# Kernel optimization log

Hardware: AMD Instinct MI355X
Metric: run time of the kernel (lower is better)

The kernel has to match this reference:

```python
import jax, jax.numpy as jnp
import numpy as np

EPS = 1e-9
ROUTING_ITERATIONS = 3


def setup_inputs() -> dict:
    key = jax.random.key(0)
    k1, k2 = jax.random.split(key)
    B, Nin, Din = 32, 2048, 16   # batch, input capsules, input capsule dim
    Nout, Dout = 64, 32          # output capsules, output capsule dim
    x = jax.random.normal(k1, (B, Nin, Din), dtype=jnp.float32)
    # transformation weights W[i, j, d, k] (shared across batch)
    W = jax.random.normal(k2, (Nin, Nout, Dout, Din), dtype=jnp.float32) * 0.05
    bias = jnp.zeros((Nout, Dout), dtype=jnp.float32)
    return {"x": x, "W": W, "bias": bias}


def _squash(s):
    # squash along last axis (capsule vector dim)
    sq_norm = jnp.sum(jnp.square(s), axis=-1, keepdims=True)
    scale = sq_norm / (1.0 + sq_norm)
    return scale * s / jnp.sqrt(sq_norm + EPS)


def reference(x, W, bias):
    # u_hat[b,i,j,d] = sum_k W[i,j,d,k] * x[b,i,k]
    u_hat = jnp.einsum('ijdk,bik->bijd', W, x)
    B, Nin, Nout, Dout = u_hat.shape
    b_log = jnp.zeros((B, Nin, Nout), dtype=u_hat.dtype)  # routing logits
    v = None
    for it in range(ROUTING_ITERATIONS):
        c = jax.nn.softmax(b_log, axis=2)                 # coupling coeffs over Nout
        s = jnp.einsum('bij,bijd->bjd', c, u_hat) + bias  # [B, Nout, Dout]
        v = _squash(s)
        if it < ROUTING_ITERATIONS - 1:
            b_log = b_log + jnp.einsum('bijd,bjd->bij', u_hat, v)
    return v  # [B, Nout, Dout]
```

## Files before the change

### kernel.cpp

```cpp
#include <hip/hip_runtime.h>
#include <hip/hip_bf16.h>
#include <stdint.h>


#define CB    32
#define NIN   2048
#define DIN   16
#define NOUT  64
#define DOUT  32
#define IPB   8
#define NCB   (NIN / IPB)
#define WI    (NOUT * DOUT * DIN)
#define WELEM ((size_t)NIN * WI)

typedef __attribute__((ext_vector_type(8)))  short bf16x8;
typedef __attribute__((ext_vector_type(16))) float f32x16;
typedef _Float16 h2 __attribute__((ext_vector_type(2)));

#define VOFF 0
#define COFF 135168
#define XOFF_IT 143616
#define SMEM_IT  153856
#define SMEM_P0  10240

static __device__ __forceinline__ uint32_t pack_bf2(float a, float b) {
    __hip_bfloat162 hh = __float22bfloat162_rn(make_float2(a, b));
    uint32_t u; __builtin_memcpy(&u, &hh, 4); return u;
}
static __device__ __forceinline__ uint16_t f2bf(float v) {
    return (uint16_t)(pack_bf2(v, 0.f) & 0xffffu);
}
static __device__ __forceinline__ float bf2f(uint16_t u) {
    uint32_t v = (uint32_t)u << 16; float f; __builtin_memcpy(&f, &v, 4); return f;
}
static __device__ __forceinline__ uint32_t pack_h2(float a, float b) {
    h2 r; r.x = (_Float16)a; r.y = (_Float16)b;
    uint32_t u; __builtin_memcpy(&u, &r, 4); return u;
}
static __device__ __forceinline__ h2 as_h2(uint32_t u) {
    h2 r; __builtin_memcpy(&r, &u, 4); return r;
}

template <int IT>
__global__ __launch_bounds__(1024, 4) void caps_pass(
    const float* __restrict__ x, const void* __restrict__ Wv,
    uint32_t* __restrict__ WhOut,
    const float* __restrict__ v_prev, const float* __restrict__ blog_in,
    float* __restrict__ blog_out, uint16_t* __restrict__ s_partial)
{
    extern __shared__ char smem[];
    uint32_t* v_lds = (uint32_t*)(smem + VOFF);
    float*    c_lds = (float*)(smem + COFF);
    uint32_t* x_lds = (uint32_t*)(smem + (IT > 0 ? XOFF_IT : 0));

    const int cb = blockIdx.x;
    const int t  = threadIdx.x;
    const int w  = t >> 6, l = t & 63;
    const int bl = l & 31, h = l >> 5;
    const int j0 = w * 4;

    {
        const int b = t >> 5, i = (t >> 2) & 7, k4 = (t & 3) * 4;
        const float4 xv = *(const float4*)(x + ((size_t)b * NIN + cb * IPB + i) * DIN + k4);
        x_lds[(i * 32 + b) * 10 + (k4 >> 1)]     = pack_bf2(xv.x, xv.y);
        x_lds[(i * 32 + b) * 10 + (k4 >> 1) + 1] = pack_bf2(xv.z, xv.w);
    }
    if (IT > 0) {
#pragma unroll 4
        for (int rep = 0; rep < 32; ++rep) {
            const int idx = rep * 1024 + t;
            const int b = idx >> 10, j = (idx >> 4) & 63, dp = idx & 15;
            const float2 vv = *(const float2*)(v_prev + ((size_t)b * NOUT + j) * DOUT + dp * 2);
            v_lds[(j * 16 + dp) * 33 + b] = pack_h2(vv.x, vv.y);
        }
    }
    __syncthreads();

    f32x16 sacc[4];
#pragma unroll
    for (int jj = 0; jj < 4; ++jj) sacc[jj] = (f32x16)0.0f;

    const uint16_t* Wb = (const uint16_t*)Wv;
    const float*    Wf = (const float*)Wv;
    constexpr int base_dp[8] = {0, 1, 4, 5, 8, 9, 12, 13};

#pragma unroll 1
    for (int i = 0; i < IPB; ++i) {
        const int ig = cb * IPB + i;
        const size_t wbase = (size_t)ig * WI;

        bf16x8 bfr;
        {
            uint32_t uu[4];
            const uint32_t* xp = &x_lds[(i * 32 + bl) * 10 + h * 4];
            uu[0] = xp[0]; uu[1] = xp[1]; uu[2] = xp[2]; uu[3] = xp[3];
            __builtin_memcpy(&bfr, uu, 16);
        }

        if (IT > 0) {
#pragma unroll
            for (int jj = 0; jj < 4; ++jj) {
                const int j = j0 + jj;
                const bf16x8 afr = *(const bf16x8*)(Wb + wbase + (size_t)(j * 32 + bl) * 16 + h * 8);
                const f32x16 D = __builtin_amdgcn_mfma_f32_32x32x16_bf16(afr, bfr, (f32x16)0.0f, 0, 0, 0);
                float acc = 0.f;
#pragma unroll
                for (int rp = 0; rp < 8; ++rp) {
                    const int dp = base_dp[rp] + 2 * h;
                    h2 dpk; dpk.x = (_Float16)D[2 * rp]; dpk.y = (_Float16)D[2 * rp + 1];
                    acc = __builtin_amdgcn_fdot2(dpk, as_h2(v_lds[(j * 16 + dp) * 33 + bl]), acc, false);
                }
                acc += __shfl_xor(acc, 32);
                if (h == 0) c_lds[j * 33 + bl] = acc;
            }
            __syncthreads();

#pragma unroll
            for (int rr = 0; rr < 2; ++rr) {
                const int b = w * 2 + rr;
                float bv = c_lds[l * 33 + b];
                if (IT == 2) bv += blog_in[((size_t)b * NIN + ig) * NOUT + l];
                if (IT == 1) blog_out[((size_t)b * NIN + ig) * NOUT + l] = bv;
                float m = bv;
#pragma unroll
                for (int o = 32; o; o >>= 1) m = fmaxf(m, __shfl_xor(m, o));
                const float e = __expf(bv - m);
                float s = e;
#pragma unroll
                for (int o = 32; o; o >>= 1) s += __shfl_xor(s, o);
                c_lds[l * 33 + b] = e / s;
            }
            __syncthreads();
        }

#pragma unroll
        for (int jj = 0; jj < 4; ++jj) {
            const int j = j0 + jj;
            if (IT == 0) {
                const float4* wp = (const float4*)(Wf + wbase + (size_t)(j * 32 + bl) * 16 + h * 8);
                const float4 a4 = wp[0], b4 = wp[1];
                uint32_t uu[4];
                uu[0] = pack_bf2(a4.x, a4.y); uu[1] = pack_bf2(a4.z, a4.w);
                uu[2] = pack_bf2(b4.x, b4.y); uu[3] = pack_bf2(b4.z, b4.w);
                bf16x8 afr; __builtin_memcpy(&afr, uu, 16);
                uint4 st; st.x = uu[0]; st.y = uu[1]; st.z = uu[2]; st.w = uu[3];
                *(uint4*)(WhOut + ((wbase + (size_t)(j * 32 + bl) * 16 + h * 8) >> 1)) = st;
                sacc[jj] = __builtin_amdgcn_mfma_f32_32x32x16_bf16(afr, bfr, sacc[jj], 0, 0, 0);
            } else {
                const bf16x8 afr = *(const bf16x8*)(Wb + wbase + (size_t)(j * 32 + bl) * 16 + h * 8);
                const f32x16 D = __builtin_amdgcn_mfma_f32_32x32x16_bf16(afr, bfr, (f32x16)0.0f, 0, 0, 0);
                const float cv = c_lds[j * 33 + bl];
                sacc[jj] += D * cv;
            }
        }
        if (IT > 0) __syncthreads();
    }

    const float cscale = (IT == 0) ? (1.0f / 64.0f) : 1.0f;
#pragma unroll
    for (int jj = 0; jj < 4; ++jj) {
        const int j = j0 + jj;
#pragma unroll
        for (int r = 0; r < 16; ++r) {
            const int d = (r & 3) + 8 * (r >> 2) + 4 * h;
            s_partial[(size_t)cb * (2048 * 32) + (size_t)(j * 32 + d) * 32 + bl] =
                f2bf(sacc[jj][r] * cscale);
        }
    }
}

__global__ __launch_bounds__(256) void caps_squash(
    const uint16_t* __restrict__ sp, const float* __restrict__ bias,
    float* __restrict__ vout)
{
    const int j  = blockIdx.x >> 2;
    const int bq = blockIdx.x & 3;
    const int t  = threadIdx.x;
    const int d  = t >> 3;
    const int blq = t & 7;
    const int b  = bq * 8 + blq;

    const uint16_t* p = sp + (size_t)(j * 32 + d) * 32 + b;
    float s0 = 0.f, s1 = 0.f, s2 = 0.f, s3 = 0.f;
#pragma unroll 4
    for (int c = 0; c < NCB; c += 4) {
        s0 += bf2f(p[(size_t)(c + 0) * (2048 * 32)]);
        s1 += bf2f(p[(size_t)(c + 1) * (2048 * 32)]);
        s2 += bf2f(p[(size_t)(c + 2) * (2048 * 32)]);
        s3 += bf2f(p[(size_t)(c + 3) * (2048 * 32)]);
    }
    const float sv = ((s0 + s1) + (s2 + s3)) + bias[j * DOUT + d];

    float sq = sv * sv;
    sq += __shfl_xor(sq, 8);
    sq += __shfl_xor(sq, 16);
    sq += __shfl_xor(sq, 32);

    __shared__ float sh[4][8];
    if ((t & 63) < 8) sh[t >> 6][t & 7] = sq;
    __syncthreads();
    const float tot = sh[0][blq] + sh[1][blq] + sh[2][blq] + sh[3][blq];
    const float scale = (tot / (1.0f + tot)) * rsqrtf(tot + 1e-9f);
    vout[(size_t)b * (NOUT * DOUT) + j * DOUT + d] = scale * sv;
}

extern "C" void kernel_launch(void* const* d_in, const int* in_sizes, int n_in,
                              void* d_out, int out_size, void* d_ws, size_t ws_size,
                              hipStream_t stream) {
    const float* x    = (const float*)d_in[0];
    const float* W    = (const float*)d_in[1];
    const float* bias = (const float*)d_in[2];
    float* out = (float*)d_out;

    char* base = (char*)d_ws;
    uint32_t* Wh    = (uint32_t*)base;
    float*    blog  = (float*)(base + WELEM * 2);
    uint16_t* spart = (uint16_t*)(base + WELEM * 2 + (size_t)CB * NIN * NOUT * 4);
    float*    vbuf  = (float*)(base + WELEM * 2 + (size_t)CB * NIN * NOUT * 4
                               + (size_t)NCB * 2048 * 32 * 2);
    (void)ws_size;

    hipFuncSetAttribute(reinterpret_cast<const void*>(caps_pass<0>),
                        hipFuncAttributeMaxDynamicSharedMemorySize, SMEM_P0);
    hipFuncSetAttribute(reinterpret_cast<const void*>(caps_pass<1>),
                        hipFuncAttributeMaxDynamicSharedMemorySize, SMEM_IT);
    hipFuncSetAttribute(reinterpret_cast<const void*>(caps_pass<2>),
                        hipFuncAttributeMaxDynamicSharedMemorySize, SMEM_IT);

    caps_pass<0><<<NCB, 1024, SMEM_P0, stream>>>(x, W, Wh, nullptr, nullptr, nullptr, spart);
    caps_squash<<<NOUT * 4, 256, 0, stream>>>(spart, bias, vbuf);

    caps_pass<1><<<NCB, 1024, SMEM_IT, stream>>>(x, Wh, nullptr, vbuf, nullptr, blog, spart);
    caps_squash<<<NOUT * 4, 256, 0, stream>>>(spart, bias, vbuf);

    caps_pass<2><<<NCB, 1024, SMEM_IT, stream>>>(x, Wh, nullptr, vbuf, blog, nullptr, spart);
    caps_squash<<<NOUT * 4, 256, 0, stream>>>(spart, bias, out);
}
```

Measured before the change: 249.2 us.

## Restructure routing passes into phased agreement, batched softmax, and scaled-x MFMA

Splits the templated pass into a separate first-pass kernel and a routing-iteration kernel. The iteration kernel now keeps v in registers instead of a large LDS table. It computes agreement logits for all 8 input capsules before doing a single softmax phase, which replaces the three barriers per input capsule with two in total. The weighted sum folds the coupling coefficient into the x operand (c*x in bf16), so the MFMA accumulates directly instead of doing a separate D*c multiply. LDS use drops from about 150KB to about 78KB, which may allow more blocks per CU. In exchange, the bf16 weights are read twice per block and rounding c*x to bf16 adds precision error.

```diff
diff --git a/kernel.cpp b/kernel.cpp
--- a/kernel.cpp
+++ b/kernel.cpp
@@ -17,11 +17,9 @@
 typedef __attribute__((ext_vector_type(16))) float f32x16;
 typedef _Float16 h2 __attribute__((ext_vector_type(2)));
 
-#define VOFF 0
-#define COFF 135168
-#define XOFF_IT 143616
-#define SMEM_IT  153856
-#define SMEM_P0  10240
+#define XOFF_IT 67584
+#define SMEM_IT 77824
+#define SMEM_P0 10240
 
 static __device__ __forceinline__ uint32_t pack_bf2(float a, float b) {
     __hip_bfloat162 hh = __float22bfloat162_rn(make_float2(a, b));
@@ -40,18 +38,19 @@
 static __device__ __forceinline__ h2 as_h2(uint32_t u) {
     h2 r; __builtin_memcpy(&r, &u, 4); return r;
 }
-
-template <int IT>
-__global__ __launch_bounds__(1024, 4) void caps_pass(
-    const float* __restrict__ x, const void* __restrict__ Wv,
-    uint32_t* __restrict__ WhOut,
-    const float* __restrict__ v_prev, const float* __restrict__ blog_in,
-    float* __restrict__ blog_out, uint16_t* __restrict__ s_partial)
+static __device__ __forceinline__ float bflo(uint32_t u) {
+    uint32_t v = u << 16; float f; __builtin_memcpy(&f, &v, 4); return f;
+}
+static __device__ __forceinline__ float bfhi(uint32_t u) {
+    uint32_t v = u & 0xffff0000u; float f; __builtin_memcpy(&f, &v, 4); return f;
+}
+
+__global__ __launch_bounds__(1024, 4) void caps_pass0(
+    const float* __restrict__ x, const float* __restrict__ Wf,
+    uint32_t* __restrict__ WhOut, uint16_t* __restrict__ s_partial)
 {
     extern __shared__ char smem[];
-    uint32_t* v_lds = (uint32_t*)(smem + VOFF);
-    float*    c_lds = (float*)(smem + COFF);
-    uint32_t* x_lds = (uint32_t*)(smem + (IT > 0 ? XOFF_IT : 0));
+    uint32_t* x_lds = (uint32_t*)smem;
 
     const int cb = blockIdx.x;
     const int t  = threadIdx.x;
@@ -65,30 +64,15 @@
         x_lds[(i * 32 + b) * 10 + (k4 >> 1)]     = pack_bf2(xv.x, xv.y);
         x_lds[(i * 32 + b) * 10 + (k4 >> 1) + 1] = pack_bf2(xv.z, xv.w);
     }
-    if (IT > 0) {
-#pragma unroll 4
-        for (int rep = 0; rep < 32; ++rep) {
-            const int idx = rep * 1024 + t;
-            const int b = idx >> 10, j = (idx >> 4) & 63, dp = idx & 15;
-            const float2 vv = *(const float2*)(v_prev + ((size_t)b * NOUT + j) * DOUT + dp * 2);
-            v_lds[(j * 16 + dp) * 33 + b] = pack_h2(vv.x, vv.y);
-        }
-    }
     __syncthreads();
 
     f32x16 sacc[4];
 #pragma unroll
     for (int jj = 0; jj < 4; ++jj) sacc[jj] = (f32x16)0.0f;
-
-    const uint16_t* Wb = (const uint16_t*)Wv;
-    const float*    Wf = (const float*)Wv;
-    constexpr int base_dp[8] = {0, 1, 4, 5, 8, 9, 12, 13};
 
 #pragma unroll 1
     for (int i = 0; i < IPB; ++i) {
-        const int ig = cb * IPB + i;
-        const size_t wbase = (size_t)ig * WI;
-
+        const size_t wbase = (size_t)(cb * IPB + i) * WI;
         bf16x8 bfr;
         {
             uint32_t uu[4];
@@ -96,67 +80,22 @@
             uu[0] = xp[0]; uu[1] = xp[1]; uu[2] = xp[2]; uu[3] = xp[3];
             __builtin_memcpy(&bfr, uu, 16);
         }
-
-        if (IT > 0) {
-#pragma unroll
-            for (int jj = 0; jj < 4; ++jj) {
-                const int j = j0 + jj;
-                const bf16x8 afr = *(const bf16x8*)(Wb + wbase + (size_t)(j * 32 + bl) * 16 + h * 8);
-                const f32x16 D = __builtin_amdgcn_mfma_f32_32x32x16_bf16(afr, bfr, (f32x16)0.0f, 0, 0, 0);
-                float acc = 0.f;
-#pragma unroll
-                for (int rp = 0; rp < 8; ++rp) {
-                    const int dp = base_dp[rp] + 2 * h;
-                    h2 dpk; dpk.x = (_Float16)D[2 * rp]; dpk.y = (_Float16)D[2 * rp + 1];
-                    acc = __builtin_amdgcn_fdot2(dpk, as_h2(v_lds[(j * 16 + dp) * 33 + bl]), acc, false);
-                }
-                acc += __shfl_xor(acc, 32);
-                if (h == 0) c_lds[j * 33 + bl] = acc;
-            }
-            __syncthreads();
-
-#pragma unroll
-            for (int rr = 0; rr < 2; ++rr) {
-                const int b = w * 2 + rr;
-                float bv = c_lds[l * 33 + b];
-                if (IT == 2) bv += blog_in[((size_t)b * NIN + ig) * NOUT + l];
-                if (IT == 1) blog_out[((size_t)b * NIN + ig) * NOUT + l] = bv;
-                float m = bv;
-#pragma unroll
-                for (int o = 32; o; o >>= 1) m = fmaxf(m, __shfl_xor(m, o));
-                const float e = __expf(bv - m);
-                float s = e;
-#pragma unroll
-                for (int o = 32; o; o >>= 1) s += __shfl_xor(s, o);
-                c_lds[l * 33 + b] = e / s;
-            }
-            __syncthreads();
-        }
-
 #pragma unroll
         for (int jj = 0; jj < 4; ++jj) {
             const int j = j0 + jj;
-            if (IT == 0) {
-                const float4* wp = (const float4*)(Wf + wbase + (size_t)(j * 32 + bl) * 16 + h * 8);
-                const float4 a4 = wp[0], b4 = wp[1];
-                uint32_t uu[4];
-                uu[0] = pack_bf2(a4.x, a4.y); uu[1] = pack_bf2(a4.z, a4.w);
-                uu[2] = pack_bf2(b4.x, b4.y); uu[3] = pack_bf2(b4.z, b4.w);
-                bf16x8 afr; __builtin_memcpy(&afr, uu, 16);
-                uint4 st; st.x = uu[0]; st.y = uu[1]; st.z = uu[2]; st.w = uu[3];
-                *(uint4*)(WhOut + ((wbase + (size_t)(j * 32 + bl) * 16 + h * 8) >> 1)) = st;
-                sacc[jj] = __builtin_amdgcn_mfma_f32_32x32x16_bf16(afr, bfr, sacc[jj], 0, 0, 0);
-            } else {
-                const bf16x8 afr = *(const bf16x8*)(Wb + wbase + (size_t)(j * 32 + bl) * 16 + h * 8);
-                const f32x16 D = __builtin_amdgcn_mfma_f32_32x32x16_bf16(afr, bfr, (f32x16)0.0f, 0, 0, 0);
-                const float cv = c_lds[j * 33 + bl];
-                sacc[jj] += D * cv;
-            }
-        }
-        if (IT > 0) __syncthreads();
-    }
-
-    const float cscale = (IT == 0) ? (1.0f / 64.0f) : 1.0f;
+            const size_t eoff = wbase + (size_t)(j * 32 + bl) * 16 + h * 8;
+            const float4* wp = (const float4*)(Wf + eoff);
+            const float4 a4 = wp[0], b4 = wp[1];
+            uint32_t uu[4];
+            uu[0] = pack_bf2(a4.x, a4.y); uu[1] = pack_bf2(a4.z, a4.w);
+            uu[2] = pack_bf2(b4.x, b4.y); uu[3] = pack_bf2(b4.z, b4.w);
+            bf16x8 afr; __builtin_memcpy(&afr, uu, 16);
+            uint4 st; st.x = uu[0]; st.y = uu[1]; st.z = uu[2]; st.w = uu[3];
+            *(uint4*)(WhOut + (eoff >> 1)) = st;
+            sacc[jj] = __builtin_amdgcn_mfma_f32_32x32x16_bf16(afr, bfr, sacc[jj], 0, 0, 0);
+        }
+    }
+
 #pragma unroll
     for (int jj = 0; jj < 4; ++jj) {
         const int j = j0 + jj;
@@ -164,7 +103,127 @@
         for (int r = 0; r < 16; ++r) {
             const int d = (r & 3) + 8 * (r >> 2) + 4 * h;
             s_partial[(size_t)cb * (2048 * 32) + (size_t)(j * 32 + d) * 32 + bl] =
-                f2bf(sacc[jj][r] * cscale);
+                f2bf(sacc[jj][r] * (1.0f / 64.0f));
+        }
+    }
+}
+
+template <int IT>
+__global__ __launch_bounds__(1024, 4) void caps_it(
+    const float* __restrict__ x, const uint16_t* __restrict__ Wh,
+    const float* __restrict__ v_prev, const float* __restrict__ blog_in,
+    float* __restrict__ blog_out, uint16_t* __restrict__ s_partial)
+{
+    extern __shared__ char smem[];
+    float*    c_lds = (float*)smem;
+    uint32_t* x_lds = (uint32_t*)(smem + XOFF_IT);
+
+    const int cb = blockIdx.x;
+    const int t  = threadIdx.x;
+    const int w  = t >> 6, l = t & 63;
+    const int bl = l & 31, h = l >> 5;
+    const int j0 = w * 4;
+
+    {
+        const int b = t >> 5, i = (t >> 2) & 7, k4 = (t & 3) * 4;
+        const float4 xv = *(const float4*)(x + ((size_t)b * NIN + cb * IPB + i) * DIN + k4);
+        x_lds[(i * 32 + b) * 10 + (k4 >> 1)]     = pack_bf2(xv.x, xv.y);
+        x_lds[(i * 32 + b) * 10 + (k4 >> 1) + 1] = pack_bf2(xv.z, xv.w);
+    }
+
+    constexpr int base_dp[8] = {0, 1, 4, 5, 8, 9, 12, 13};
+    uint32_t vreg[4][8];
+#pragma unroll
+    for (int jj = 0; jj < 4; ++jj)
+#pragma unroll
+        for (int rp = 0; rp < 8; ++rp) {
+            const int d0 = 2 * (base_dp[rp] + 2 * h);
+            const float2 vv = *(const float2*)(v_prev
+                + ((size_t)bl * NOUT + j0 + jj) * DOUT + d0);
+            vreg[jj][rp] = pack_h2(vv.x, vv.y);
+        }
+    __syncthreads();
+
+#pragma unroll 2
+    for (int i = 0; i < IPB; ++i) {
+        const size_t wbase = (size_t)(cb * IPB + i) * WI;
+        bf16x8 bfr;
+        {
+            uint32_t uu[4];
+            const uint32_t* xp = &x_lds[(i * 32 + bl) * 10 + h * 4];
+            uu[0] = xp[0]; uu[1] = xp[1]; uu[2] = xp[2]; uu[3] = xp[3];
+            __builtin_memcpy(&bfr, uu, 16);
+        }
+#pragma unroll
+        for (int jj = 0; jj < 4; ++jj) {
+            const int j = j0 + jj;
+            const bf16x8 afr = *(const bf16x8*)(Wh + wbase + (size_t)(j * 32 + bl) * 16 + h * 8);
+            const f32x16 D = __builtin_amdgcn_mfma_f32_32x32x16_bf16(afr, bfr, (f32x16)0.0f, 0, 0, 0);
+            float acc = 0.f;
+#pragma unroll
+            for (int rp = 0; rp < 8; ++rp) {
+                h2 dpk; dpk.x = (_Float16)D[2 * rp]; dpk.y = (_Float16)D[2 * rp + 1];
+                acc = __builtin_amdgcn_fdot2(dpk, as_h2(vreg[jj][rp]), acc, false);
+            }
+            acc += __shfl_xor(acc, 32);
+            if (h == 0) c_lds[(i * 64 + j) * 33 + bl] = acc;
+        }
+    }
+    __syncthreads();
+
+#pragma unroll 1
+    for (int q = 0; q < 16; ++q) {
+        const int row = w * 16 + q;
+        const int i = row >> 5, b = row & 31;
+        const int ig = cb * IPB + i;
+        float bv = c_lds[(i * 64 + l) * 33 + b];
+        if (IT == 2) bv += blog_in[((size_t)b * NIN + ig) * NOUT + l];
+        if (IT == 1) blog_out[((size_t)b * NIN + ig) * NOUT + l] = bv;
+        float m = bv;
+#pragma unroll
+        for (int o = 32; o; o >>= 1) m = fmaxf(m, __shfl_xor(m, o));
+        const float e = __expf(bv - m);
+        float s = e;
+#pragma unroll
+        for (int o = 32; o; o >>= 1) s += __shfl_xor(s, o);
+        c_lds[(i * 64 + l) * 33 + b] = e / s;
+    }
+    __syncthreads();
+
+    f32x16 sacc[4];
+#pragma unroll
+    for (int jj = 0; jj < 4; ++jj) sacc[jj] = (f32x16)0.0f;
+
+#pragma unroll 2
+    for (int i = 0; i < IPB; ++i) {
+        const size_t wbase = (size_t)(cb * IPB + i) * WI;
+        uint32_t xu[4];
+        {
+            const uint32_t* xp = &x_lds[(i * 32 + bl) * 10 + h * 4];
+            xu[0] = xp[0]; xu[1] = xp[1]; xu[2] = xp[2]; xu[3] = xp[3];
+        }
+#pragma unroll
+        for (int jj = 0; jj < 4; ++jj) {
+            const int j = j0 + jj;
+            const bf16x8 afr = *(const bf16x8*)(Wh + wbase + (size_t)(j * 32 + bl) * 16 + h * 8);
+            const float cv = c_lds[(i * 64 + j) * 33 + bl];
+            uint32_t cu[4];
+#pragma unroll
+            for (int q = 0; q < 4; ++q)
+                cu[q] = pack_bf2(bflo(xu[q]) * cv, bfhi(xu[q]) * cv);
+            bf16x8 cxf; __builtin_memcpy(&cxf, cu, 16);
+            sacc[jj] = __builtin_amdgcn_mfma_f32_32x32x16_bf16(afr, cxf, sacc[jj], 0, 0, 0);
+        }
+    }
+
+#pragma unroll
+    for (int jj = 0; jj < 4; ++jj) {
+        const int j = j0 + jj;
+#pragma unroll
+        for (int r = 0; r < 16; ++r) {
+            const int d = (r & 3) + 8 * (r >> 2) + 4 * h;
+            s_partial[(size_t)cb * (2048 * 32) + (size_t)(j * 32 + d) * 32 + bl] =
+                f2bf(sacc[jj][r]);
         }
     }
 }
@@ -220,19 +279,19 @@
                                + (size_t)NCB * 2048 * 32 * 2);
     (void)ws_size;
 
-    hipFuncSetAttribute(reinterpret_cast<const void*>(caps_pass<0>),
+    hipFuncSetAttribute(reinterpret_cast<const void*>(caps_pass0),
                         hipFuncAttributeMaxDynamicSharedMemorySize, SMEM_P0);
-    hipFuncSetAttribute(reinterpret_cast<const void*>(caps_pass<1>),
+    hipFuncSetAttribute(reinterpret_cast<const void*>(caps_it<1>),
                         hipFuncAttributeMaxDynamicSharedMemorySize, SMEM_IT);
-    hipFuncSetAttribute(reinterpret_cast<const void*>(caps_pass<2>),
+    hipFuncSetAttribute(reinterpret_cast<const void*>(caps_it<2>),
                         hipFuncAttributeMaxDynamicSharedMemorySize, SMEM_IT);
 
-    caps_pass<0><<<NCB, 1024, SMEM_P0, stream>>>(x, W, Wh, nullptr, nullptr, nullptr, spart);
+    caps_pass0<<<NCB, 1024, SMEM_P0, stream>>>(x, W, (uint32_t*)Wh, spart);
     caps_squash<<<NOUT * 4, 256, 0, stream>>>(spart, bias, vbuf);
 
-    caps_pass<1><<<NCB, 1024, SMEM_IT, stream>>>(x, Wh, nullptr, vbuf, nullptr, blog, spart);
+    caps_it<1><<<NCB, 1024, SMEM_IT, stream>>>(x, (const uint16_t*)Wh, vbuf, nullptr, blog, spart);
     caps_squash<<<NOUT * 4, 256, 0, stream>>>(spart, bias, vbuf);
 
-    caps_pass<2><<<NCB, 1024, SMEM_IT, stream>>>(x, Wh, nullptr, vbuf, blog, nullptr, spart);
+    caps_it<2><<<NCB, 1024, SMEM_IT, stream>>>(x, (const uint16_t*)Wh, vbuf, blog, nullptr, spart);
     caps_squash<<<NOUT * 4, 256, 0, stream>>>(spart, bias, out);
 }
```

After: 261.8 us. +5.1%, slower.
